# Optimization experiments

Hardware: AMD Instinct MI355X
Metric: run time of the kernel (lower is better)

The kernel has to match this reference:

```python
import jax, jax.numpy as jnp
import numpy as np

N_NODES = 20000
N_EDGES = 400000
IN_DIM = 512
OUT_DIM = 1
HIDDEN = [512, 512, 512, 256, OUT_DIM]


def _glorot(key, fan_in, fan_out):
    lim = np.sqrt(6.0 / (fan_in + fan_out)).astype(np.float32)
    return jax.random.uniform(key, (fan_in, fan_out), jnp.float32, -lim, lim)


def setup_inputs() -> dict:
    key = jax.random.key(0)
    ks = jax.random.split(key, 16)
    x = jax.random.normal(ks[0], (N_NODES, IN_DIM), jnp.float32)
    edge_index = jax.random.randint(ks[1], (2, N_EDGES), 0, N_NODES, jnp.int64)
    edge_attr = jax.random.uniform(ks[2], (N_EDGES,), jnp.float32)
    inp = {"x": x, "edge_index": edge_index, "edge_attr": edge_attr}
    dims = [IN_DIM] + HIDDEN
    for i in range(5):
        inp[f"W{i+1}"] = _glorot(ks[3 + i], dims[i], dims[i + 1])
        inp[f"b{i+1}"] = jnp.zeros((dims[i + 1],), jnp.float32)
    return inp


def gcn_layer(x, W, b, src, dst, ew, n):
    # x: [N, Fin] -> [N, Fout]; GCNConv: D^{-1/2}(A+I)D^{-1/2} X W + b
    h = x @ W
    loop = jnp.arange(n)
    src_f = jnp.concatenate([src, loop])
    dst_f = jnp.concatenate([dst, loop])
    ew_f = jnp.concatenate([ew, jnp.ones((n,), x.dtype)])  # self-loop weight 1
    deg = jax.ops.segment_sum(ew_f, dst_f, num_segments=n)
    dinv = jnp.where(deg > 0, jax.lax.rsqrt(deg), 0.0)
    norm = dinv[src_f] * ew_f * dinv[dst_f]  # [E+N]
    out = jax.ops.segment_sum(norm[:, None] * h[src_f], dst_f, num_segments=n)
    return out + b


def reference(x, edge_index, edge_attr, W1, b1, W2, b2, W3, b3, W4, b4, W5, b5):
    src, dst = edge_index[0], edge_index[1]
    n = x.shape[0]
    h = jax.nn.relu(gcn_layer(x, W1, b1, src, dst, edge_attr, n))
    h = jax.nn.relu(gcn_layer(h, W2, b2, src, dst, edge_attr, n))
    h = jax.nn.relu(gcn_layer(h, W3, b3, src, dst, edge_attr, n))
    h = jax.nn.relu(gcn_layer(h, W4, b4, src, dst, edge_attr, n))
    h = gcn_layer(h, W5, b5, src, dst, edge_attr, n)
    return h
```

## Files before the change

kernel.cpp:

```cpp
#include <hip/hip_runtime.h>
#include <cstdint>
#include <cstddef>

#define N_NODES 20000
#define N_EDGES 400000
#define NBLK 79
#define MPAD 20128

typedef __attribute__((ext_vector_type(8))) short bf16x8;
typedef __attribute__((ext_vector_type(4))) float f32x4;
typedef __attribute__((ext_vector_type(2))) int i32x2;

__device__ __forceinline__ float bf2f(unsigned short u) {
    return __uint_as_float(((unsigned int)u) << 16);
}
__device__ __forceinline__ unsigned short f2bf(float f) {
    unsigned int x = __float_as_uint(f);
    unsigned int lsb = (x >> 16) & 1u;
    x += 0x7fffu + lsb;
    return (unsigned short)(x >> 16);
}

__device__ __forceinline__ float ldF(const void* p, size_t i, bool bf) {
    return bf ? bf2f(((const unsigned short*)p)[i]) : ((const float*)p)[i];
}

__device__ __forceinline__ void gl2lds16(const unsigned short* g, unsigned short* l) {
    __builtin_amdgcn_global_load_lds(
        (const __attribute__((address_space(1))) void*)g,
        (__attribute__((address_space(3))) void*)l, 16, 0, 0);
}

__global__ void k_detect(const unsigned int* __restrict__ xw, const int* __restrict__ raw,
                         int* __restrict__ flag) {
    int lane = threadIdx.x;
    int cnt = 0, nz = 0;
    for (int i = lane; i < 256; i += 64) {
        unsigned short lo = (unsigned short)(xw[i] & 0xffffu);
        int e = (lo >> 7) & 0xff;
        if (e >= 110 && e <= 135) cnt++;
    }
    for (int i = 2 * lane + 1; i < 512; i += 128)
        if (raw[i] != 0) nz++;
#pragma unroll
    for (int off = 32; off > 0; off >>= 1) {
        cnt += __shfl_down(cnt, off);
        nz  += __shfl_down(nz, off);
    }
    if (lane == 0) {
        flag[0] = (cnt >= 128) ? 1 : 0;
        flag[1] = (nz == 0) ? 1 : 0;
    }
}

__global__ void k_canon_deg(const int* __restrict__ raw, const void* __restrict__ ew,
                            const int* __restrict__ flagp,
                            float* __restrict__ deg, int* __restrict__ counts) {
    bool bf = (flagp[0] != 0);
    int is64 = flagp[1];
    int e = blockIdx.x * blockDim.x + threadIdx.x;
    if (e >= N_EDGES) return;
    int d;
    if (is64) d = raw[2 * (N_EDGES + e)];
    else      d = raw[N_EDGES + e];
    atomicAdd(&deg[d], ldF(ew, e, bf));
    atomicAdd(&counts[d], 1);
}

__global__ __launch_bounds__(256) void k_part(const int* __restrict__ counts,
                                              const float* __restrict__ deg,
                                              float* __restrict__ dinv,
                                              float* __restrict__ selfnorm,
                                              int* __restrict__ bsum) {
    __shared__ int s[256];
    int t = threadIdx.x;
    int i = blockIdx.x * 256 + t;
    int c = (i < N_NODES) ? counts[i] : 0;
    if (i < N_NODES) {
        float d = deg[i] + 1.0f;
        float r = rsqrtf(d);
        dinv[i] = r;
        selfnorm[i] = r * r;
    }
    s[t] = c;
    __syncthreads();
    for (int off = 128; off > 0; off >>= 1) {
        if (t < off) s[t] += s[t + off];
        __syncthreads();
    }
    if (t == 0) bsum[blockIdx.x] = s[0];
}

__global__ void k_scanb(const int* __restrict__ bsum, int* __restrict__ bofs,
                        int* __restrict__ rowptr) {
    __shared__ int s[128];
    int t = threadIdx.x;
    int v = (t < NBLK) ? bsum[t] : 0;
    s[t] = v;
    __syncthreads();
    for (int off = 1; off < 128; off <<= 1) {
        int u = (t >= off) ? s[t - off] : 0;
        __syncthreads();
        s[t] += u;
        __syncthreads();
    }
    if (t < NBLK) bofs[t] = s[t] - v;
    if (t == NBLK - 1) rowptr[N_NODES] = s[t];
}

__global__ __launch_bounds__(256) void k_row(const int* __restrict__ counts,
                                             const int* __restrict__ bofs,
                                             int* __restrict__ rowptr) {
    __shared__ int s[256];
    int t = threadIdx.x;
    int b = blockIdx.x;
    int i = b * 256 + t;
    int c = (i < N_NODES) ? counts[i] : 0;
    s[t] = c;
    __syncthreads();
    for (int off = 1; off < 256; off <<= 1) {
        int u = (t >= off) ? s[t - off] : 0;
        __syncthreads();
        s[t] += u;
        __syncthreads();
    }
    if (i < N_NODES) rowptr[i] = bofs[b] + s[t] - c;
}

__global__ void k_csr(const int* __restrict__ raw, const void* __restrict__ ew,
                      const int* __restrict__ flagp,
                      const float* __restrict__ dinv, const int* __restrict__ rowptr,
                      int* __restrict__ fill, int* __restrict__ csr_pair) {
    bool bf = (flagp[0] != 0);
    int is64 = flagp[1];
    int e = blockIdx.x * blockDim.x + threadIdx.x;
    if (e >= N_EDGES) return;
    int s, d;
    if (is64) { s = raw[2 * e]; d = raw[2 * (N_EDGES + e)]; }
    else      { s = raw[e];     d = raw[N_EDGES + e]; }
    int p = rowptr[d] + atomicAdd(&fill[d], 1);
    float nrm = dinv[s] * ldF(ew, e, bf) * dinv[d];
    i32x2 pv;
    pv.x = s;
    pv.y = __float_as_int(nrm);
    *(i32x2*)(csr_pair + 2 * (size_t)p) = pv;
}

__global__ __launch_bounds__(256) void k_prep(const void* __restrict__ x,
                                              const void* __restrict__ W1,
                                              const void* __restrict__ W2,
                                              const void* __restrict__ W3,
                                              const void* __restrict__ W4,
                                              const void* __restrict__ b1,
                                              const void* __restrict__ b2,
                                              const void* __restrict__ b3,
                                              const void* __restrict__ b4,
                                              const void* __restrict__ W5,
                                              const int* __restrict__ flagp,
                                              unsigned short* __restrict__ P,
                                              unsigned short* __restrict__ Wp,
                                              float* __restrict__ biasf) {
    bool bf = (*flagp != 0);
    int b = blockIdx.x;
    int t = threadIdx.x;
    if (b < 10000) {
        if (bf) return;
        int i = b * 256 + t;
        float4 v = ((const float4*)x)[i];
        unsigned int lo = (unsigned int)f2bf(v.x) | ((unsigned int)f2bf(v.y) << 16);
        unsigned int hi = (unsigned int)f2bf(v.z) | ((unsigned int)f2bf(v.w) << 16);
        ((uint2*)P)[i] = make_uint2(lo, hi);
    } else if (b < 10448) {
        int gidx = (b - 10000) * 256 + t;
        if (gidx >= 114688) return;
        const void* W;
        int idx = gidx, N, nbl;
        if (gidx < 32768)      { W = W1; N = 512; nbl = 5; }
        else if (gidx < 65536) { W = W2; N = 512; nbl = 5; idx -= 32768; }
        else if (gidx < 98304) { W = W3; N = 512; nbl = 5; idx -= 65536; }
        else                   { W = W4; N = 256; nbl = 4; idx -= 98304; }
        int lane = idx & 63;
        int blk = idx >> 6;
        int nb = blk & ((1 << nbl) - 1);
        int kb = blk >> nbl;
        int n = (nb << 4) + (lane & 15);
        int kbase = (kb << 5) + ((lane >> 4) << 3);
        unsigned short o[8];
#pragma unroll
        for (int j = 0; j < 8; ++j)
            o[j] = f2bf(ldF(W, (size_t)(kbase + j) * N + n, bf));
        *(uint4*)(&Wp[(size_t)gidx * 8]) = *(const uint4*)o;
    } else {
        int i = (b - 10448) * 256 + t;
        if (i >= 2304) return;
        if (i < 2048) {
            int L = i >> 9, r = i & 511;
            if (L == 3 && r >= 256) return;
            const void* bb = (L == 0) ? b1 : (L == 1) ? b2 : (L == 2) ? b3 : b4;
            biasf[i] = ldF(bb, r, bf);
        } else {
            biasf[i] = ldF(W5, i - 2048, bf);
        }
    }
}

__global__ __launch_bounds__(256) void k_gemm_mfma(const unsigned short* __restrict__ Abase,
                                                   const unsigned short* __restrict__ Aalt,
                                                   const int* __restrict__ flagp,
                                                   const unsigned short* __restrict__ Bp,
                                                   unsigned short* __restrict__ C,
                                                   int M, int K, int N) {
    const int AP = 72;
    __shared__ __align__(16) unsigned short As[128 * AP];
    __shared__ __align__(16) unsigned short Bs[2 * 8 * 512];
    const unsigned short* A = (*flagp != 0) ? Aalt : Abase;
    int tid = threadIdx.x;
    int lane = tid & 63;
    int wave = tid >> 6;
    int wr = wave >> 1, wc = wave & 1;
    int row0 = blockIdx.x * 128;
    int col0 = blockIdx.y * 128;
    int nbt = N >> 4;
    int q = lane >> 4;
    int mm = lane & 15;

    f32x4 acc[4][4] = {};

    for (int kb2 = 0; kb2 < (K >> 6); ++kb2) {
        const unsigned short* breg0 = Bp + (((size_t)(2 * kb2) * nbt + (col0 >> 4)) << 9);
        const unsigned short* breg1 = Bp + (((size_t)(2 * kb2 + 1) * nbt + (col0 >> 4)) << 9);
        gl2lds16(breg0 + (size_t)tid * 8, &Bs[(size_t)tid * 8]);
        gl2lds16(breg0 + (size_t)(tid + 256) * 8, &Bs[(size_t)(tid + 256) * 8]);
        gl2lds16(breg1 + (size_t)tid * 8, &Bs[4096 + (size_t)tid * 8]);
        gl2lds16(breg1 + (size_t)(tid + 256) * 8, &Bs[4096 + (size_t)(tid + 256) * 8]);
#pragma unroll
        for (int i = 0; i < 4; ++i) {
            int c = tid + i * 256;
            int row = c >> 3, kq = c & 7;
            int grow = min(row0 + row, M - 1);
            uint4 v = *(const uint4*)(&A[(size_t)grow * K + (kb2 << 6) + (kq << 3)]);
            *(uint4*)(&As[row * AP + (kq << 3)]) = v;
        }
        __syncthreads();
#pragma unroll
        for (int kk = 0; kk < 2; ++kk) {
            bf16x8 af[4], bfr[4];
#pragma unroll
            for (int mb = 0; mb < 4; ++mb)
                af[mb] = *(const bf16x8*)(&As[(wr * 64 + mb * 16 + mm) * AP + kk * 32 + q * 8]);
#pragma unroll
            for (int nb = 0; nb < 4; ++nb)
                bfr[nb] = *(const bf16x8*)(&Bs[kk * 4096 + ((wc * 4 + nb) * 64 + lane) * 8]);
#pragma unroll
            for (int mb = 0; mb < 4; ++mb)
#pragma unroll
                for (int nb = 0; nb < 4; ++nb)
                    acc[mb][nb] = __builtin_amdgcn_mfma_f32_16x16x32_bf16(
                        af[mb], bfr[nb], acc[mb][nb], 0, 0, 0);
        }
        __syncthreads();
    }
#pragma unroll
    for (int mb = 0; mb < 4; ++mb) {
#pragma unroll
        for (int r = 0; r < 4; ++r) {
            int grow = row0 + wr * 64 + mb * 16 + q * 4 + r;
            if (grow < M) {
#pragma unroll
                for (int nb = 0; nb < 4; ++nb) {
                    int gcol = col0 + wc * 64 + nb * 16 + mm;
                    C[(size_t)grow * N + gcol] = f2bf(acc[mb][nb][r]);
                }
            }
        }
    }
}

template <int W>
__device__ __forceinline__ void ldrow(const unsigned short* h, size_t row, int F, int lane,
                                      unsigned int* u) {
    const unsigned int* p = (const unsigned int*)(h + row * F) + lane * W;
    if constexpr (W == 4) {
        uint4 v = *(const uint4*)p; u[0] = v.x; u[1] = v.y; u[2] = v.z; u[3] = v.w;
    } else {
        uint2 v = *(const uint2*)p; u[0] = v.x; u[1] = v.y;
    }
}
template <int W>
__device__ __forceinline__ void fmarow(const unsigned int* u, float w, float* acc) {
#pragma unroll
    for (int k = 0; k < W; ++k) {
        acc[2 * k]     = fmaf(bf2f((unsigned short)(u[k] & 0xffffu)), w, acc[2 * k]);
        acc[2 * k + 1] = fmaf(bf2f((unsigned short)(u[k] >> 16)),     w, acc[2 * k + 1]);
    }
}

__global__ __launch_bounds__(64) void k_agg_w(const unsigned short* __restrict__ h,
                                              const int* __restrict__ rowptr,
                                              const int* __restrict__ csr_pair,
                                              const float* __restrict__ selfnorm,
                                              const float* __restrict__ biasf,
                                              unsigned short* __restrict__ out) {
    constexpr int F = 512;
    int tid = threadIdx.x;
    int half = tid >> 5;
    int col = tid & 31;
    int chunk = blockIdx.x & 7;
    int node = (blockIdx.x >> 3) * 2 + half;
    int e0 = rowptr[node], e1 = rowptr[node + 1];
    float sn = selfnorm[node];
    const unsigned short* hb = h + chunk * 64 + col * 2;

    float a0, a1;
    {
        unsigned int u = *(const unsigned int*)(hb + (size_t)node * F);
        a0 = sn * bf2f((unsigned short)(u & 0xffffu));
        a1 = sn * bf2f((unsigned short)(u >> 16));
    }
    const i32x2* pairs = (const i32x2*)csr_pair;
    int j = e0;
    for (; j + 7 < e1; j += 8) {
        i32x2 p0 = pairs[j],     p1 = pairs[j + 1], p2 = pairs[j + 2], p3 = pairs[j + 3];
        i32x2 p4 = pairs[j + 4], p5 = pairs[j + 5], p6 = pairs[j + 6], p7 = pairs[j + 7];
        unsigned int u0 = *(const unsigned int*)(hb + (size_t)p0.x * F);
        unsigned int u1 = *(const unsigned int*)(hb + (size_t)p1.x * F);
        unsigned int u2 = *(const unsigned int*)(hb + (size_t)p2.x * F);
        unsigned int u3 = *(const unsigned int*)(hb + (size_t)p3.x * F);
        unsigned int u4 = *(const unsigned int*)(hb + (size_t)p4.x * F);
        unsigned int u5 = *(const unsigned int*)(hb + (size_t)p5.x * F);
        unsigned int u6 = *(const unsigned int*)(hb + (size_t)p6.x * F);
        unsigned int u7 = *(const unsigned int*)(hb + (size_t)p7.x * F);
        float w0 = __int_as_float(p0.y), w1 = __int_as_float(p1.y);
        float w2 = __int_as_float(p2.y), w3 = __int_as_float(p3.y);
        float w4 = __int_as_float(p4.y), w5 = __int_as_float(p5.y);
        float w6 = __int_as_float(p6.y), w7 = __int_as_float(p7.y);
        a0 = fmaf(bf2f((unsigned short)(u0 & 0xffffu)), w0, a0);
        a1 = fmaf(bf2f((unsigned short)(u0 >> 16)),     w0, a1);
        a0 = fmaf(bf2f((unsigned short)(u1 & 0xffffu)), w1, a0);
        a1 = fmaf(bf2f((unsigned short)(u1 >> 16)),     w1, a1);
        a0 = fmaf(bf2f((unsigned short)(u2 & 0xffffu)), w2, a0);
        a1 = fmaf(bf2f((unsigned short)(u2 >> 16)),     w2, a1);
        a0 = fmaf(bf2f((unsigned short)(u3 & 0xffffu)), w3, a0);
        a1 = fmaf(bf2f((unsigned short)(u3 >> 16)),     w3, a1);
        a0 = fmaf(bf2f((unsigned short)(u4 & 0xffffu)), w4, a0);
        a1 = fmaf(bf2f((unsigned short)(u4 >> 16)),     w4, a1);
        a0 = fmaf(bf2f((unsigned short)(u5 & 0xffffu)), w5, a0);
        a1 = fmaf(bf2f((unsigned short)(u5 >> 16)),     w5, a1);
        a0 = fmaf(bf2f((unsigned short)(u6 & 0xffffu)), w6, a0);
        a1 = fmaf(bf2f((unsigned short)(u6 >> 16)),     w6, a1);
        a0 = fmaf(bf2f((unsigned short)(u7 & 0xffffu)), w7, a0);
        a1 = fmaf(bf2f((unsigned short)(u7 >> 16)),     w7, a1);
    }
    for (; j + 3 < e1; j += 4) {
        i32x2 p0 = pairs[j], p1 = pairs[j + 1], p2 = pairs[j + 2], p3 = pairs[j + 3];
        unsigned int u0 = *(const unsigned int*)(hb + (size_t)p0.x * F);
        unsigned int u1 = *(const unsigned int*)(hb + (size_t)p1.x * F);
        unsigned int u2 = *(const unsigned int*)(hb + (size_t)p2.x * F);
        unsigned int u3 = *(const unsigned int*)(hb + (size_t)p3.x * F);
        float w0 = __int_as_float(p0.y), w1 = __int_as_float(p1.y);
        float w2 = __int_as_float(p2.y), w3 = __int_as_float(p3.y);
        a0 = fmaf(bf2f((unsigned short)(u0 & 0xffffu)), w0, a0);
        a1 = fmaf(bf2f((unsigned short)(u0 >> 16)),     w0, a1);
        a0 = fmaf(bf2f((unsigned short)(u1 & 0xffffu)), w1, a0);
        a1 = fmaf(bf2f((unsigned short)(u1 >> 16)),     w1, a1);
        a0 = fmaf(bf2f((unsigned short)(u2 & 0xffffu)), w2, a0);
        a1 = fmaf(bf2f((unsigned short)(u2 >> 16)),     w2, a1);
        a0 = fmaf(bf2f((unsigned short)(u3 & 0xffffu)), w3, a0);
        a1 = fmaf(bf2f((unsigned short)(u3 >> 16)),     w3, a1);
    }
    for (; j < e1; ++j) {
        i32x2 p0 = pairs[j];
        unsigned int u0 = *(const unsigned int*)(hb + (size_t)p0.x * F);
        float w0 = __int_as_float(p0.y);
        a0 = fmaf(bf2f((unsigned short)(u0 & 0xffffu)), w0, a0);
        a1 = fmaf(bf2f((unsigned short)(u0 >> 16)),     w0, a1);
    }
    {
        const float* bp = biasf + chunk * 64 + col * 2;
        a0 = fmaxf(a0 + bp[0], 0.f);
        a1 = fmaxf(a1 + bp[1], 0.f);
        unsigned int o = (unsigned int)f2bf(a0) | ((unsigned int)f2bf(a1) << 16);
        *(unsigned int*)(out + (size_t)node * F + chunk * 64 + col * 2) = o;
    }
}

__global__ __launch_bounds__(64) void k_agg_fuse(const unsigned short* __restrict__ h,
                                                 const int* __restrict__ rowptr,
                                                 const int* __restrict__ csr_pair,
                                                 const float* __restrict__ selfnorm,
                                                 const float* __restrict__ biasf,
                                                 const float* __restrict__ w5f,
                                                 float* __restrict__ h5) {
    constexpr int F = 256, FPL = 4, W = 2;
    int lane = threadIdx.x;
    int node = blockIdx.x;
    int e0 = rowptr[node], e1 = rowptr[node + 1];
    float sn = selfnorm[node];

    float acc[FPL];
    {
        unsigned int u[W];
        ldrow<W>(h, (size_t)node, F, lane, u);
#pragma unroll
        for (int k = 0; k < W; ++k) {
            acc[2 * k]     = sn * bf2f((unsigned short)(u[k] & 0xffffu));
            acc[2 * k + 1] = sn * bf2f((unsigned short)(u[k] >> 16));
        }
    }
    const i32x2* pairs = (const i32x2*)csr_pair;
    int j = e0;
    for (; j + 7 < e1; j += 8) {
        i32x2 p0 = pairs[j],     p1 = pairs[j + 1], p2 = pairs[j + 2], p3 = pairs[j + 3];
        i32x2 p4 = pairs[j + 4], p5 = pairs[j + 5], p6 = pairs[j + 6], p7 = pairs[j + 7];
        unsigned int u0[W], u1[W], u2[W], u3[W], u4[W], u5[W], u6[W], u7[W];
        ldrow<W>(h, (size_t)p0.x, F, lane, u0);
        ldrow<W>(h, (size_t)p1.x, F, lane, u1);
        ldrow<W>(h, (size_t)p2.x, F, lane, u2);
        ldrow<W>(h, (size_t)p3.x, F, lane, u3);
        ldrow<W>(h, (size_t)p4.x, F, lane, u4);
        ldrow<W>(h, (size_t)p5.x, F, lane, u5);
        ldrow<W>(h, (size_t)p6.x, F, lane, u6);
        ldrow<W>(h, (size_t)p7.x, F, lane, u7);
        fmarow<W>(u0, __int_as_float(p0.y), acc);
        fmarow<W>(u1, __int_as_float(p1.y), acc);
        fmarow<W>(u2, __int_as_float(p2.y), acc);
        fmarow<W>(u3, __int_as_float(p3.y), acc);
        fmarow<W>(u4, __int_as_float(p4.y), acc);
        fmarow<W>(u5, __int_as_float(p5.y), acc);
        fmarow<W>(u6, __int_as_float(p6.y), acc);
        fmarow<W>(u7, __int_as_float(p7.y), acc);
    }
    for (; j + 3 < e1; j += 4) {
        i32x2 p0 = pairs[j], p1 = pairs[j + 1], p2 = pairs[j + 2], p3 = pairs[j + 3];
        unsigned int u0[W], u1[W], u2[W], u3[W];
        ldrow<W>(h, (size_t)p0.x, F, lane, u0);
        ldrow<W>(h, (size_t)p1.x, F, lane, u1);
        ldrow<W>(h, (size_t)p2.x, F, lane, u2);
        ldrow<W>(h, (size_t)p3.x, F, lane, u3);
        fmarow<W>(u0, __int_as_float(p0.y), acc);
        fmarow<W>(u1, __int_as_float(p1.y), acc);
        fmarow<W>(u2, __int_as_float(p2.y), acc);
        fmarow<W>(u3, __int_as_float(p3.y), acc);
    }
    for (; j < e1; ++j) {
        i32x2 p0 = pairs[j];
        unsigned int u0[W];
        ldrow<W>(h, (size_t)p0.x, F, lane, u0);
        fmarow<W>(u0, __int_as_float(p0.y), acc);
    }
    const float* bp = biasf + lane * FPL;
    const float* wp = w5f + lane * FPL;
    float partial = 0.f;
#pragma unroll
    for (int k = 0; k < FPL; ++k)
        partial += fmaxf(acc[k] + bp[k], 0.f) * wp[k];
#pragma unroll
    for (int off = 32; off > 0; off >>= 1)
        partial += __shfl_xor(partial, off);
    if (lane == 0) h5[node] = partial;
}

__global__ void k_final(const float* __restrict__ h5, const int* __restrict__ rowptr,
                        const int* __restrict__ csr_pair,
                        const float* __restrict__ selfnorm,
                        const void* __restrict__ b5, const int* __restrict__ flagp,
                        void* __restrict__ out) {
    bool bf = (*flagp != 0);
    int i = blockIdx.x * blockDim.x + threadIdx.x;
    if (i >= N_NODES) return;
    float acc = selfnorm[i] * h5[i];
    int e0 = rowptr[i], e1 = rowptr[i + 1];
    for (int j = e0; j < e1; ++j) {
        int s = csr_pair[2 * (size_t)j];
        float w = __int_as_float(csr_pair[2 * (size_t)j + 1]);
        acc += w * h5[s];
    }
    acc += ldF(b5, 0, bf);
    if (bf) ((unsigned short*)out)[i] = f2bf(acc);
    else    ((float*)out)[i] = acc;
}

extern "C" void kernel_launch(void* const* d_in, const int* in_sizes, int n_in,
                              void* d_out, int out_size, void* d_ws, size_t ws_size,
                              hipStream_t stream) {
    const void* x  = d_in[0];
    const int*  ei = (const int*)d_in[1];
    const void* ea = d_in[2];
    const void* W1 = d_in[3];
    const void* b1 = d_in[4];
    const void* W2 = d_in[5];
    const void* b2 = d_in[6];
    const void* W3 = d_in[7];
    const void* b3 = d_in[8];
    const void* W4 = d_in[9];
    const void* b4 = d_in[10];
    const void* W5 = d_in[11];
    const void* b5 = d_in[12];

    char* ws = (char*)d_ws;
    size_t off = 0;
    auto take = [&](size_t bytes) -> void* {
        off = (off + 255) & ~(size_t)255;
        void* p = ws + off;
        off += bytes;
        return p;
    };
    int*   flagp    = (int*)take(2 * sizeof(int));
    float* deg      = (float*)take(N_NODES * sizeof(float));
    int*   counts   = (int*)take(N_NODES * sizeof(int));
    int*   fill     = (int*)take(N_NODES * sizeof(int));
    size_t zspan    = (size_t)((char*)(fill + N_NODES) - (char*)deg);
    float* dinv     = (float*)take(N_NODES * sizeof(float));
    float* selfnorm = (float*)take(N_NODES * sizeof(float));
    float* h5       = (float*)take(N_NODES * sizeof(float));
    float* biasf    = (float*)take(2304 * sizeof(float));
    int*   bsum     = (int*)take(128 * sizeof(int));
    int*   bofs     = (int*)take(128 * sizeof(int));
    int*   rowptr   = (int*)take((N_NODES + 1) * sizeof(int));
    int*   csr_pair = (int*)take((size_t)N_EDGES * 2 * sizeof(int));
    unsigned short* Wp = (unsigned short*)take((size_t)114688 * 8 * sizeof(unsigned short));
    unsigned short* P  = (unsigned short*)take((size_t)MPAD * 512 * sizeof(unsigned short));
    unsigned short* H  = (unsigned short*)take((size_t)MPAD * 512 * sizeof(unsigned short));

    (void)hipMemsetAsync(deg, 0, zspan, stream);

    const int EB = (N_EDGES + 255) / 256;
    const int NB = (N_NODES + 255) / 256;
    const int AGW = (N_NODES / 2) * 8;

    k_detect<<<1, 64, 0, stream>>>((const unsigned int*)x, ei, flagp);
    k_canon_deg<<<EB, 256, 0, stream>>>(ei, ea, flagp, deg, counts);
    k_part<<<NB, 256, 0, stream>>>(counts, deg, dinv, selfnorm, bsum);
    k_scanb<<<1, 128, 0, stream>>>(bsum, bofs, rowptr);
    k_row<<<NB, 256, 0, stream>>>(counts, bofs, rowptr);
    k_csr<<<EB, 256, 0, stream>>>(ei, ea, flagp, dinv, rowptr, fill, csr_pair);

    k_prep<<<10457, 256, 0, stream>>>(x, W1, W2, W3, W4, b1, b2, b3, b4, W5, flagp,
                                      P, Wp, biasf);

    const int MB128 = (N_NODES + 127) / 128;

    k_gemm_mfma<<<dim3(MB128, 4), 256, 0, stream>>>(P, (const unsigned short*)x, flagp,
                                                    Wp, H, N_NODES, 512, 512);
    k_agg_w<<<AGW, 64, 0, stream>>>(H, rowptr, csr_pair, selfnorm, biasf, P);
    k_gemm_mfma<<<dim3(MB128, 4), 256, 0, stream>>>(P, P, flagp,
                                                    Wp + (size_t)32768 * 8, H,
                                                    N_NODES, 512, 512);
    k_agg_w<<<AGW, 64, 0, stream>>>(H, rowptr, csr_pair, selfnorm, biasf + 512, P);
    k_gemm_mfma<<<dim3(MB128, 4), 256, 0, stream>>>(P, P, flagp,
                                                    Wp + (size_t)65536 * 8, H,
                                                    N_NODES, 512, 512);
    k_agg_w<<<AGW, 64, 0, stream>>>(H, rowptr, csr_pair, selfnorm, biasf + 1024, P);
    k_gemm_mfma<<<dim3(MB128, 2), 256, 0, stream>>>(P, P, flagp,
                                                    Wp + (size_t)98304 * 8, H,
                                                    N_NODES, 512, 256);
    k_agg_fuse<<<N_NODES, 64, 0, stream>>>(H, rowptr, csr_pair, selfnorm,
                                           biasf + 1536, biasf + 2048, h5);

    k_final<<<NB, 256, 0, stream>>>(h5, rowptr, csr_pair, selfnorm, b5, flagp,
                                    d_out);
}
```

Before: 479.9 us.

## Split each node's edge list across two half-waves and reduce via shuffle

Aggregation kernels now assign one 64-lane block per node-chunk, with each 32-lane half processing alternating edges and combining partial sums through a cross-half shuffle. This replaces the previous two-nodes-per-block mapping in which each half handled a different node. The fused layer-4 kernel is split into 4 column chunks per node and accumulates into h5 with atomics, so h5 is now zeroed by the existing memset. The aim is shorter per-node serial chains and more parallelism for the gather loops. The cost is twice as many blocks, extra shuffles and atomics, and more reads of the pair array.

```diff
diff --git a/kernel.cpp b/kernel.cpp
--- a/kernel.cpp
+++ b/kernel.cpp
@@ -276,25 +276,6 @@
     }
 }
 
-template <int W>
-__device__ __forceinline__ void ldrow(const unsigned short* h, size_t row, int F, int lane,
-                                      unsigned int* u) {
-    const unsigned int* p = (const unsigned int*)(h + row * F) + lane * W;
-    if constexpr (W == 4) {
-        uint4 v = *(const uint4*)p; u[0] = v.x; u[1] = v.y; u[2] = v.z; u[3] = v.w;
-    } else {
-        uint2 v = *(const uint2*)p; u[0] = v.x; u[1] = v.y;
-    }
-}
-template <int W>
-__device__ __forceinline__ void fmarow(const unsigned int* u, float w, float* acc) {
-#pragma unroll
-    for (int k = 0; k < W; ++k) {
-        acc[2 * k]     = fmaf(bf2f((unsigned short)(u[k] & 0xffffu)), w, acc[2 * k]);
-        acc[2 * k + 1] = fmaf(bf2f((unsigned short)(u[k] >> 16)),     w, acc[2 * k + 1]);
-    }
-}
-
 __global__ __launch_bounds__(64) void k_agg_w(const unsigned short* __restrict__ h,
                                               const int* __restrict__ rowptr,
                                               const int* __restrict__ csr_pair,
@@ -306,13 +287,13 @@
     int half = tid >> 5;
     int col = tid & 31;
     int chunk = blockIdx.x & 7;
-    int node = (blockIdx.x >> 3) * 2 + half;
+    int node = blockIdx.x >> 3;
     int e0 = rowptr[node], e1 = rowptr[node + 1];
-    float sn = selfnorm[node];
     const unsigned short* hb = h + chunk * 64 + col * 2;
 
-    float a0, a1;
-    {
+    float a0 = 0.f, a1 = 0.f;
+    if (half == 0) {
+        float sn = selfnorm[node];
         unsigned int u = *(const unsigned int*)(hb + (size_t)node * F);
         a0 = sn * bf2f((unsigned short)(u & 0xffffu));
         a1 = sn * bf2f((unsigned short)(u >> 16));
@@ -320,20 +301,22 @@
     const i32x2* pairs = (const i32x2*)csr_pair;
     int j = e0;
     for (; j + 7 < e1; j += 8) {
-        i32x2 p0 = pairs[j],     p1 = pairs[j + 1], p2 = pairs[j + 2], p3 = pairs[j + 3];
-        i32x2 p4 = pairs[j + 4], p5 = pairs[j + 5], p6 = pairs[j + 6], p7 = pairs[j + 7];
-        unsigned int u0 = *(const unsigned int*)(hb + (size_t)p0.x * F);
-        unsigned int u1 = *(const unsigned int*)(hb + (size_t)p1.x * F);
-        unsigned int u2 = *(const unsigned int*)(hb + (size_t)p2.x * F);
-        unsigned int u3 = *(const unsigned int*)(hb + (size_t)p3.x * F);
-        unsigned int u4 = *(const unsigned int*)(hb + (size_t)p4.x * F);
-        unsigned int u5 = *(const unsigned int*)(hb + (size_t)p5.x * F);
-        unsigned int u6 = *(const unsigned int*)(hb + (size_t)p6.x * F);
-        unsigned int u7 = *(const unsigned int*)(hb + (size_t)p7.x * F);
-        float w0 = __int_as_float(p0.y), w1 = __int_as_float(p1.y);
-        float w2 = __int_as_float(p2.y), w3 = __int_as_float(p3.y);
-        float w4 = __int_as_float(p4.y), w5 = __int_as_float(p5.y);
-        float w6 = __int_as_float(p6.y), w7 = __int_as_float(p7.y);
+        i32x2 q0 = pairs[j],     q1 = pairs[j + 1];
+        i32x2 q2 = pairs[j + 2], q3 = pairs[j + 3];
+        i32x2 q4 = pairs[j + 4], q5 = pairs[j + 5];
+        i32x2 q6 = pairs[j + 6], q7 = pairs[j + 7];
+        int   s0 = half ? q1.x : q0.x;
+        int   s1 = half ? q3.x : q2.x;
+        int   s2 = half ? q5.x : q4.x;
+        int   s3 = half ? q7.x : q6.x;
+        float w0 = __int_as_float(half ? q1.y : q0.y);
+        float w1 = __int_as_float(half ? q3.y : q2.y);
+        float w2 = __int_as_float(half ? q5.y : q4.y);
+        float w3 = __int_as_float(half ? q7.y : q6.y);
+        unsigned int u0 = *(const unsigned int*)(hb + (size_t)s0 * F);
+        unsigned int u1 = *(const unsigned int*)(hb + (size_t)s1 * F);
+        unsigned int u2 = *(const unsigned int*)(hb + (size_t)s2 * F);
+        unsigned int u3 = *(const unsigned int*)(hb + (size_t)s3 * F);
         a0 = fmaf(bf2f((unsigned short)(u0 & 0xffffu)), w0, a0);
         a1 = fmaf(bf2f((unsigned short)(u0 >> 16)),     w0, a1);
         a0 = fmaf(bf2f((unsigned short)(u1 & 0xffffu)), w1, a0);
@@ -342,23 +325,70 @@
         a1 = fmaf(bf2f((unsigned short)(u2 >> 16)),     w2, a1);
         a0 = fmaf(bf2f((unsigned short)(u3 & 0xffffu)), w3, a0);
         a1 = fmaf(bf2f((unsigned short)(u3 >> 16)),     w3, a1);
-        a0 = fmaf(bf2f((unsigned short)(u4 & 0xffffu)), w4, a0);
-        a1 = fmaf(bf2f((unsigned short)(u4 >> 16)),     w4, a1);
-        a0 = fmaf(bf2f((unsigned short)(u5 & 0xffffu)), w5, a0);
-        a1 = fmaf(bf2f((unsigned short)(u5 >> 16)),     w5, a1);
-        a0 = fmaf(bf2f((unsigned short)(u6 & 0xffffu)), w6, a0);
-        a1 = fmaf(bf2f((unsigned short)(u6 >> 16)),     w6, a1);
-        a0 = fmaf(bf2f((unsigned short)(u7 & 0xffffu)), w7, a0);
-        a1 = fmaf(bf2f((unsigned short)(u7 >> 16)),     w7, a1);
-    }
-    for (; j + 3 < e1; j += 4) {
-        i32x2 p0 = pairs[j], p1 = pairs[j + 1], p2 = pairs[j + 2], p3 = pairs[j + 3];
-        unsigned int u0 = *(const unsigned int*)(hb + (size_t)p0.x * F);
-        unsigned int u1 = *(const unsigned int*)(hb + (size_t)p1.x * F);
-        unsigned int u2 = *(const unsigned int*)(hb + (size_t)p2.x * F);
-        unsigned int u3 = *(const unsigned int*)(hb + (size_t)p3.x * F);
-        float w0 = __int_as_float(p0.y), w1 = __int_as_float(p1.y);
-        float w2 = __int_as_float(p2.y), w3 = __int_as_float(p3.y);
+    }
+    for (; j < e1; j += 2) {
+        i32x2 q0 = pairs[j];
+        i32x2 q1 = pairs[min(j + 1, e1 - 1)];
+        bool ok1 = (j + 1) < e1;
+        int   s0 = half ? q1.x : q0.x;
+        float w0 = half ? (ok1 ? __int_as_float(q1.y) : 0.f) : __int_as_float(q0.y);
+        unsigned int u0 = *(const unsigned int*)(hb + (size_t)s0 * F);
+        a0 = fmaf(bf2f((unsigned short)(u0 & 0xffffu)), w0, a0);
+        a1 = fmaf(bf2f((unsigned short)(u0 >> 16)),     w0, a1);
+    }
+    a0 += __shfl_xor(a0, 32);
+    a1 += __shfl_xor(a1, 32);
+    if (half == 0) {
+        const float* bp = biasf + chunk * 64 + col * 2;
+        a0 = fmaxf(a0 + bp[0], 0.f);
+        a1 = fmaxf(a1 + bp[1], 0.f);
+        unsigned int o = (unsigned int)f2bf(a0) | ((unsigned int)f2bf(a1) << 16);
+        *(unsigned int*)(out + (size_t)node * F + chunk * 64 + col * 2) = o;
+    }
+}
+
+__global__ __launch_bounds__(64) void k_agg_fuse(const unsigned short* __restrict__ h,
+                                                 const int* __restrict__ rowptr,
+                                                 const int* __restrict__ csr_pair,
+                                                 const float* __restrict__ selfnorm,
+                                                 const float* __restrict__ biasf,
+                                                 const float* __restrict__ w5f,
+                                                 float* __restrict__ h5) {
+    constexpr int F = 256;
+    int tid = threadIdx.x;
+    int half = tid >> 5;
+    int col = tid & 31;
+    int chunk = blockIdx.x & 3;
+    int node = blockIdx.x >> 2;
+    int e0 = rowptr[node], e1 = rowptr[node + 1];
+    const unsigned short* hb = h + chunk * 64 + col * 2;
+
+    float a0 = 0.f, a1 = 0.f;
+    if (half == 0) {
+        float sn = selfnorm[node];
+        unsigned int u = *(const unsigned int*)(hb + (size_t)node * F);
+        a0 = sn * bf2f((unsigned short)(u & 0xffffu));
+        a1 = sn * bf2f((unsigned short)(u >> 16));
+    }
+    const i32x2* pairs = (const i32x2*)csr_pair;
+    int j = e0;
+    for (; j + 7 < e1; j += 8) {
+        i32x2 q0 = pairs[j],     q1 = pairs[j + 1];
+        i32x2 q2 = pairs[j + 2], q3 = pairs[j + 3];
+        i32x2 q4 = pairs[j + 4], q5 = pairs[j + 5];
+        i32x2 q6 = pairs[j + 6], q7 = pairs[j + 7];
+        int   s0 = half ? q1.x : q0.x;
+        int   s1 = half ? q3.x : q2.x;
+        int   s2 = half ? q5.x : q4.x;
+        int   s3 = half ? q7.x : q6.x;
+        float w0 = __int_as_float(half ? q1.y : q0.y);
+        float w1 = __int_as_float(half ? q3.y : q2.y);
+        float w2 = __int_as_float(half ? q5.y : q4.y);
+        float w3 = __int_as_float(half ? q7.y : q6.y);
+        unsigned int u0 = *(const unsigned int*)(hb + (size_t)s0 * F);
+        unsigned int u1 = *(const unsigned int*)(hb + (size_t)s1 * F);
+        unsigned int u2 = *(const unsigned int*)(hb + (size_t)s2 * F);
+        unsigned int u3 = *(const unsigned int*)(hb + (size_t)s3 * F);
         a0 = fmaf(bf2f((unsigned short)(u0 & 0xffffu)), w0, a0);
         a1 = fmaf(bf2f((unsigned short)(u0 >> 16)),     w0, a1);
         a0 = fmaf(bf2f((unsigned short)(u1 & 0xffffu)), w1, a0);
@@ -368,96 +398,30 @@
         a0 = fmaf(bf2f((unsigned short)(u3 & 0xffffu)), w3, a0);
         a1 = fmaf(bf2f((unsigned short)(u3 >> 16)),     w3, a1);
     }
-    for (; j < e1; ++j) {
-        i32x2 p0 = pairs[j];
-        unsigned int u0 = *(const unsigned int*)(hb + (size_t)p0.x * F);
-        float w0 = __int_as_float(p0.y);
+    for (; j < e1; j += 2) {
+        i32x2 q0 = pairs[j];
+        i32x2 q1 = pairs[min(j + 1, e1 - 1)];
+        bool ok1 = (j + 1) < e1;
+        int   s0 = half ? q1.x : q0.x;
+        float w0 = half ? (ok1 ? __int_as_float(q1.y) : 0.f) : __int_as_float(q0.y);
+        unsigned int u0 = *(const unsigned int*)(hb + (size_t)s0 * F);
         a0 = fmaf(bf2f((unsigned short)(u0 & 0xffffu)), w0, a0);
         a1 = fmaf(bf2f((unsigned short)(u0 >> 16)),     w0, a1);
     }
-    {
+    a0 += __shfl_xor(a0, 32);
+    a1 += __shfl_xor(a1, 32);
+    if (half == 0) {
         const float* bp = biasf + chunk * 64 + col * 2;
-        a0 = fmaxf(a0 + bp[0], 0.f);
-        a1 = fmaxf(a1 + bp[1], 0.f);
-        unsigned int o = (unsigned int)f2bf(a0) | ((unsigned int)f2bf(a1) << 16);
-        *(unsigned int*)(out + (size_t)node * F + chunk * 64 + col * 2) = o;
-    }
-}
-
-__global__ __launch_bounds__(64) void k_agg_fuse(const unsigned short* __restrict__ h,
-                                                 const int* __restrict__ rowptr,
-                                                 const int* __restrict__ csr_pair,
-                                                 const float* __restrict__ selfnorm,
-                                                 const float* __restrict__ biasf,
-                                                 const float* __restrict__ w5f,
-                                                 float* __restrict__ h5) {
-    constexpr int F = 256, FPL = 4, W = 2;
-    int lane = threadIdx.x;
-    int node = blockIdx.x;
-    int e0 = rowptr[node], e1 = rowptr[node + 1];
-    float sn = selfnorm[node];
-
-    float acc[FPL];
-    {
-        unsigned int u[W];
-        ldrow<W>(h, (size_t)node, F, lane, u);
-#pragma unroll
-        for (int k = 0; k < W; ++k) {
-            acc[2 * k]     = sn * bf2f((unsigned short)(u[k] & 0xffffu));
-            acc[2 * k + 1] = sn * bf2f((unsigned short)(u[k] >> 16));
-        }
-    }
-    const i32x2* pairs = (const i32x2*)csr_pair;
-    int j = e0;
-    for (; j + 7 < e1; j += 8) {
-        i32x2 p0 = pairs[j],     p1 = pairs[j + 1], p2 = pairs[j + 2], p3 = pairs[j + 3];
-        i32x2 p4 = pairs[j + 4], p5 = pairs[j + 5], p6 = pairs[j + 6], p7 = pairs[j + 7];
-        unsigned int u0[W], u1[W], u2[W], u3[W], u4[W], u5[W], u6[W], u7[W];
-        ldrow<W>(h, (size_t)p0.x, F, lane, u0);
-        ldrow<W>(h, (size_t)p1.x, F, lane, u1);
-        ldrow<W>(h, (size_t)p2.x, F, lane, u2);
-        ldrow<W>(h, (size_t)p3.x, F, lane, u3);
-        ldrow<W>(h, (size_t)p4.x, F, lane, u4);
-        ldrow<W>(h, (size_t)p5.x, F, lane, u5);
-        ldrow<W>(h, (size_t)p6.x, F, lane, u6);
-        ldrow<W>(h, (size_t)p7.x, F, lane, u7);
-        fmarow<W>(u0, __int_as_float(p0.y), acc);
-        fmarow<W>(u1, __int_as_float(p1.y), acc);
-        fmarow<W>(u2, __int_as_float(p2.y), acc);
-        fmarow<W>(u3, __int_as_float(p3.y), acc);
-        fmarow<W>(u4, __int_as_float(p4.y), acc);
-        fmarow<W>(u5, __int_as_float(p5.y), acc);
-        fmarow<W>(u6, __int_as_float(p6.y), acc);
-        fmarow<W>(u7, __int_as_float(p7.y), acc);
-    }
-    for (; j + 3 < e1; j += 4) {
-        i32x2 p0 = pairs[j], p1 = pairs[j + 1], p2 = pairs[j + 2], p3 = pairs[j + 3];
-        unsigned int u0[W], u1[W], u2[W], u3[W];
-        ldrow<W>(h, (size_t)p0.x, F, lane, u0);
-        ldrow<W>(h, (size_t)p1.x, F, lane, u1);
-        ldrow<W>(h, (size_t)p2.x, F, lane, u2);
-        ldrow<W>(h, (size_t)p3.x, F, lane, u3);
-        fmarow<W>(u0, __int_as_float(p0.y), acc);
-        fmarow<W>(u1, __int_as_float(p1.y), acc);
-        fmarow<W>(u2, __int_as_float(p2.y), acc);
-        fmarow<W>(u3, __int_as_float(p3.y), acc);
-    }
-    for (; j < e1; ++j) {
-        i32x2 p0 = pairs[j];
-        unsigned int u0[W];
-        ldrow<W>(h, (size_t)p0.x, F, lane, u0);
-        fmarow<W>(u0, __int_as_float(p0.y), acc);
-    }
-    const float* bp = biasf + lane * FPL;
-    const float* wp = w5f + lane * FPL;
-    float partial = 0.f;
-#pragma unroll
-    for (int k = 0; k < FPL; ++k)
-        partial += fmaxf(acc[k] + bp[k], 0.f) * wp[k];
-#pragma unroll
-    for (int off = 32; off > 0; off >>= 1)
-        partial += __shfl_xor(partial, off);
-    if (lane == 0) h5[node] = partial;
+        const float* wp = w5f + chunk * 64 + col * 2;
+        float partial = fmaxf(a0 + bp[0], 0.f) * wp[0]
+                      + fmaxf(a1 + bp[1], 0.f) * wp[1];
+        partial += __shfl_xor(partial, 1);
+        partial += __shfl_xor(partial, 2);
+        partial += __shfl_xor(partial, 4);
+        partial += __shfl_xor(partial, 8);
+        partial += __shfl_xor(partial, 16);
+        if (col == 0) atomicAdd(h5 + node, partial);
+    }
 }
 
 __global__ void k_final(const float* __restrict__ h5, const int* __restrict__ rowptr,
@@ -509,10 +473,10 @@
     float* deg      = (float*)take(N_NODES * sizeof(float));
     int*   counts   = (int*)take(N_NODES * sizeof(int));
     int*   fill     = (int*)take(N_NODES * sizeof(int));
-    size_t zspan    = (size_t)((char*)(fill + N_NODES) - (char*)deg);
+    float* h5       = (float*)take(N_NODES * sizeof(float));
+    size_t zspan    = (size_t)((char*)(h5 + N_NODES) - (char*)deg);
     float* dinv     = (float*)take(N_NODES * sizeof(float));
     float* selfnorm = (float*)take(N_NODES * sizeof(float));
-    float* h5       = (float*)take(N_NODES * sizeof(float));
     float* biasf    = (float*)take(2304 * sizeof(float));
     int*   bsum     = (int*)take(128 * sizeof(int));
     int*   bofs     = (int*)take(128 * sizeof(int));
@@ -526,7 +490,8 @@
 
     const int EB = (N_EDGES + 255) / 256;
     const int NB = (N_NODES + 255) / 256;
-    const int AGW = (N_NODES / 2) * 8;
+    const int AGW = N_NODES * 8;
+    const int AGF = N_NODES * 4;
 
     k_detect<<<1, 64, 0, stream>>>((const unsigned int*)x, ei, flagp);
     k_canon_deg<<<EB, 256, 0, stream>>>(ei, ea, flagp, deg, counts);
@@ -554,8 +519,8 @@
     k_gemm_mfma<<<dim3(MB128, 2), 256, 0, stream>>>(P, P, flagp,
                                                     Wp + (size_t)98304 * 8, H,
                                                     N_NODES, 512, 256);
-    k_agg_fuse<<<N_NODES, 64, 0, stream>>>(H, rowptr, csr_pair, selfnorm,
-                                           biasf + 1536, biasf + 2048, h5);
+    k_agg_fuse<<<AGF, 64, 0, stream>>>(H, rowptr, csr_pair, selfnorm,
+                                       biasf + 1536, biasf + 2048, h5);
 
     k_final<<<NB, 256, 0, stream>>>(h5, rowptr, csr_pair, selfnorm, b5, flagp,
                                     d_out);
```

New measurement: 477.0 us. No clear change (-0.6%).
